# Optimization experiments

Measured on AMD Instinct MI355X. Metric: run time of the kernel, lower is better.

## Reference

```python
import jax, jax.numpy as jnp
import numpy as np

N = 20000      # nodes
E = 320000     # edges
F = 128        # feat_dim
N_RBF = 20
CUTOFF = 5.0


def setup_inputs() -> dict:
    key = jax.random.key(0)
    ks = jax.random.split(key, 12)
    h_i = jax.random.normal(ks[0], (N, F), dtype=jnp.float32)
    v_i = jax.random.normal(ks[1], (N, F, 3), dtype=jnp.float32)
    # distances in (0, cutoff); keep strictly > 0 to avoid div-by-zero in sinc basis
    d_ij = (jax.random.uniform(ks[2], (E,), dtype=jnp.float32) * 0.98 + 0.01) * CUTOFF
    r = jax.random.normal(ks[3], (E, 3), dtype=jnp.float32)
    unit_r_ij = r / jnp.linalg.norm(r, axis=-1, keepdims=True)
    nbrs = jax.random.randint(ks[4], (E, 2), 0, N, dtype=jnp.int64)
    # params: layers = Dense(F->F, swish) then Dense(F->3F); dist_embed dense: n_rbf -> 3F
    s1 = 1.0 / np.sqrt(F)
    W1 = jax.random.uniform(ks[5], (F, F), jnp.float32, -s1, s1)
    b1 = jax.random.uniform(ks[6], (F,), jnp.float32, -s1, s1)
    W2 = jax.random.uniform(ks[7], (F, 3 * F), jnp.float32, -s1, s1)
    b2 = jax.random.uniform(ks[8], (3 * F,), jnp.float32, -s1, s1)
    sr = 1.0 / np.sqrt(N_RBF)
    Wr = jax.random.uniform(ks[9], (N_RBF, 3 * F), jnp.float32, -sr, sr)
    br = jax.random.uniform(ks[10], (3 * F,), jnp.float32, -sr, sr)
    return {"h_i": h_i, "v_i": v_i, "d_ij": d_ij, "unit_r_ij": unit_r_ij,
            "nbrs": nbrs, "W1": W1, "b1": b1, "W2": W2, "b2": b2, "Wr": Wr, "br": br}


def _dist_embed(d, Wr, br):
    # PaiNN sinc-like radial basis: sin(n*pi*d/cutoff)/d, n=1..N_RBF
    n = jnp.arange(1, N_RBF + 1, dtype=d.dtype)
    rbf = jnp.sin(n[None, :] * jnp.pi * d[:, None] / CUTOFF) / d[:, None]  # [E, N_RBF]
    # cosine cutoff envelope
    fcut = 0.5 * (jnp.cos(jnp.pi * d / CUTOFF) + 1.0) * (d < CUTOFF)       # [E]
    return (rbf @ Wr + br) * fcut[:, None]                                  # [E, 3F]


def reference(h_i, v_i, d_ij, unit_r_ij, nbrs, W1, b1, W2, b2, Wr, br):
    # phi = Dense(swish) -> Dense : [N, 3F]
    phi = jax.nn.silu(h_i @ W1 + b1) @ W2 + b2
    src = nbrs[:, 1]
    dst = nbrs[:, 0]
    edge_inv = phi[src] * _dist_embed(d_ij, Wr, br)          # [E, 3F]
    edge_inv = edge_inv.reshape(edge_inv.shape[0], 3, F)     # [E, 3, F]
    f1, f2, f3 = edge_inv[:, 0], edge_inv[:, 1], edge_inv[:, 2]
    # dv: [E, F, 3]
    dv = f1[:, :, None] * unit_r_ij[:, None, :] + f2[:, :, None] * v_i[src]
    dh_i = jax.ops.segment_sum(f3, dst, num_segments=N)      # [N, F]
    dv_i = jax.ops.segment_sum(dv, dst, num_segments=N)      # [N, F, 3]
    return (dh_i, dv_i)
```

## Files before the change

kernel.cpp:

```cpp
#include <hip/hip_runtime.h>
#include <math.h>

#define F 128
#define THREEF 384
#define N_RBF 20
#define CUTOFF 5.0f
#define CAP 64

#define REP20(X) X(0) X(1) X(2) X(3) X(4) X(5) X(6) X(7) X(8) X(9) \
                 X(10) X(11) X(12) X(13) X(14) X(15) X(16) X(17) X(18) X(19)

__global__ __launch_bounds__(256) void mlp_kernel(
    const float* __restrict__ h, const float* __restrict__ W1,
    const float* __restrict__ b1, const float* __restrict__ W2,
    const float* __restrict__ b2, float* __restrict__ phi, int N)
{
    __shared__ float sh_h[16 * F];
    __shared__ float sh_t[16 * F];
    const int tid   = threadIdx.x;
    const int node0 = blockIdx.x * 16;

    {
        const float4* src = (const float4*)(h + (size_t)node0 * F);
        float4* dst = (float4*)sh_h;
        dst[tid]       = src[tid];
        dst[tid + 256] = src[tid + 256];
    }
    __syncthreads();

    const int j2 = tid & 63;
    const int r0 = (tid >> 6) * 4;

    {
        float acc[4][2];
        const float bb0 = b1[j2], bb1 = b1[j2 + 64];
        #pragma unroll
        for (int r = 0; r < 4; ++r) { acc[r][0] = bb0; acc[r][1] = bb1; }
        for (int k4 = 0; k4 < F; k4 += 4) {
            float4 a[4];
            #pragma unroll
            for (int r = 0; r < 4; ++r)
                a[r] = *(const float4*)&sh_h[(r0 + r) * F + k4];
            #pragma unroll
            for (int kk = 0; kk < 4; ++kk) {
                const float w0  = W1[(k4 + kk) * F + j2];
                const float w1v = W1[(k4 + kk) * F + j2 + 64];
                #pragma unroll
                for (int r = 0; r < 4; ++r) {
                    const float av = ((const float*)&a[r])[kk];
                    acc[r][0] = fmaf(av, w0,  acc[r][0]);
                    acc[r][1] = fmaf(av, w1v, acc[r][1]);
                }
            }
        }
        #pragma unroll
        for (int r = 0; r < 4; ++r) {
            const float x0 = acc[r][0], x1 = acc[r][1];
            sh_t[(r0 + r) * F + j2]      = x0 / (1.0f + __expf(-x0));
            sh_t[(r0 + r) * F + j2 + 64] = x1 / (1.0f + __expf(-x1));
        }
    }
    __syncthreads();

    {
        float acc[4][6];
        #pragma unroll
        for (int c = 0; c < 6; ++c) {
            const float bb = b2[j2 + c * 64];
            #pragma unroll
            for (int r = 0; r < 4; ++r) acc[r][c] = bb;
        }
        for (int k4 = 0; k4 < F; k4 += 4) {
            float4 a[4];
            #pragma unroll
            for (int r = 0; r < 4; ++r)
                a[r] = *(const float4*)&sh_t[(r0 + r) * F + k4];
            #pragma unroll
            for (int kk = 0; kk < 4; ++kk) {
                float w[6];
                #pragma unroll
                for (int c = 0; c < 6; ++c)
                    w[c] = W2[(k4 + kk) * THREEF + j2 + c * 64];
                #pragma unroll
                for (int r = 0; r < 4; ++r) {
                    const float av = ((const float*)&a[r])[kk];
                    #pragma unroll
                    for (int c = 0; c < 6; ++c)
                        acc[r][c] = fmaf(av, w[c], acc[r][c]);
                }
            }
        }
        #pragma unroll
        for (int r = 0; r < 4; ++r) {
            #pragma unroll
            for (int c = 0; c < 6; ++c) {
                const int col = j2 + c * 64;
                const int p   = col >> 7;
                const int fc  = col & 127;
                phi[(size_t)p * N * F + (size_t)(node0 + r0 + r) * F + fc] = acc[r][c];
            }
        }
    }
}

__global__ __launch_bounds__(256) void build_kernel(
    const float* __restrict__ d_ij, const float* __restrict__ unit_r,
    const int* __restrict__ nbrs, int* __restrict__ cnt,
    int* __restrict__ eid, float* __restrict__ pack, int E)
{
    int e = blockIdx.x * 256 + threadIdx.x;
    if (e >= E) return;
    const int dst = nbrs[2 * e];
    const int src = nbrs[2 * e + 1];
    const int slot = atomicAdd(&cnt[dst], 1);
    if (slot < CAP) eid[dst * CAP + slot] = e;

    const float d = d_ij[e];
    const float x = (float)M_PI * d * (1.0f / CUTOFF);
    float sx, cx;
    __sincosf(x, &sx, &cx);
    const float fcut = (d < CUTOFF) ? 0.5f * (cx + 1.0f) : 0.0f;
    float4 q0, q1;
    q0.x = sx * fcut / d;
    q0.y = 2.0f * cx;
    q0.z = fcut;
    q0.w = unit_r[3 * e + 0];
    q1.x = unit_r[3 * e + 1];
    q1.y = unit_r[3 * e + 2];
    q1.z = __int_as_float(src);
    q1.w = 0.0f;
    float4* pk = (float4*)(pack + (size_t)e * 8);
    pk[0] = q0;
    pk[1] = q1;
}

__global__ __launch_bounds__(128) void gather_kernel(
    const float* __restrict__ phi,
    const float* __restrict__ v_i,
    const float* __restrict__ Wr,
    const float* __restrict__ br,
    const int*   __restrict__ cnt,
    const int*   __restrict__ eid,
    const float* __restrict__ pack,
    float* __restrict__ dh,
    float* __restrict__ dv,
    int N)
{
    const int node = blockIdx.x;
    const int f    = threadIdx.x;

    #define DECL_WR(n) float w0_##n = Wr[(n) * THREEF + f];        \
                       float w1_##n = Wr[(n) * THREEF + f + 128];  \
                       float w2_##n = Wr[(n) * THREEF + f + 256];
    REP20(DECL_WR)
    #undef DECL_WR

    asm volatile("" : "+v"(w0_0), "+v"(w0_1), "+v"(w0_2), "+v"(w0_3),
                      "+v"(w0_4), "+v"(w0_5), "+v"(w0_6), "+v"(w0_7),
                      "+v"(w0_8), "+v"(w0_9), "+v"(w0_10), "+v"(w0_11),
                      "+v"(w0_12), "+v"(w0_13), "+v"(w0_14));
    asm volatile("" : "+v"(w0_15), "+v"(w0_16), "+v"(w0_17), "+v"(w0_18),
                      "+v"(w0_19), "+v"(w1_0), "+v"(w1_1), "+v"(w1_2),
                      "+v"(w1_3), "+v"(w1_4), "+v"(w1_5), "+v"(w1_6),
                      "+v"(w1_7), "+v"(w1_8), "+v"(w1_9));
    asm volatile("" : "+v"(w1_10), "+v"(w1_11), "+v"(w1_12), "+v"(w1_13),
                      "+v"(w1_14), "+v"(w1_15), "+v"(w1_16), "+v"(w1_17),
                      "+v"(w1_18), "+v"(w1_19), "+v"(w2_0), "+v"(w2_1),
                      "+v"(w2_2), "+v"(w2_3), "+v"(w2_4));
    asm volatile("" : "+v"(w2_5), "+v"(w2_6), "+v"(w2_7), "+v"(w2_8),
                      "+v"(w2_9), "+v"(w2_10), "+v"(w2_11), "+v"(w2_12),
                      "+v"(w2_13), "+v"(w2_14), "+v"(w2_15), "+v"(w2_16),
                      "+v"(w2_17), "+v"(w2_18), "+v"(w2_19));

    const float br0 = br[f], br1 = br[f + 128], br2 = br[f + 256];

    const int deg0 = cnt[node];
    const int deg  = deg0 < CAP ? deg0 : CAP;
    const int* my_eid = eid + node * CAP;

    const float* phi0 = phi;
    const float* phi1 = phi + (size_t)N * F;
    const float* phi2 = phi + (size_t)2 * N * F;

    float dh_acc = 0.0f, dv0 = 0.0f, dv1 = 0.0f, dv2 = 0.0f;

    for (int i = 0; i < deg; ++i) {
        const int e = __builtin_amdgcn_readfirstlane(my_eid[i]);
        const float* pk = pack + (size_t)e * 8;
        const float s1   = pk[0];
        const float twoc = pk[1];
        const float fcut = pk[2];
        const float ux   = pk[3];
        const float uy   = pk[4];
        const float uz   = pk[5];
        const int src = __builtin_amdgcn_readfirstlane(__float_as_int(pk[6]));

        float a0 = br0 * fcut, a1 = br1 * fcut, a2 = br2 * fcut;
        float rp = 0.0f, rc = s1;
        #define STEP(n) { a0 = fmaf(rc, w0_##n, a0);            \
                          a1 = fmaf(rc, w1_##n, a1);            \
                          a2 = fmaf(rc, w2_##n, a2);            \
                          const float rn = fmaf(twoc, rc, -rp); \
                          rp = rc; rc = rn; }
        REP20(STEP)
        #undef STEP

        const float f1 = phi0[(size_t)src * F + f] * a0;
        const float f2 = phi1[(size_t)src * F + f] * a1;
        const float f3 = phi2[(size_t)src * F + f] * a2;

        dh_acc += f3;

        const float* vs = v_i + (size_t)src * THREEF + 3 * f;
        dv0 = fmaf(f1, ux, fmaf(f2, vs[0], dv0));
        dv1 = fmaf(f1, uy, fmaf(f2, vs[1], dv1));
        dv2 = fmaf(f1, uz, fmaf(f2, vs[2], dv2));
    }

    dh[(size_t)node * F + f] = dh_acc;
    float* dvp = dv + (size_t)node * THREEF + 3 * f;
    dvp[0] = dv0;
    dvp[1] = dv1;
    dvp[2] = dv2;
}

extern "C" void kernel_launch(void* const* d_in, const int* in_sizes, int n_in,
                              void* d_out, int out_size, void* d_ws, size_t ws_size,
                              hipStream_t stream) {
    const float* h_i    = (const float*)d_in[0];
    const float* v_i    = (const float*)d_in[1];
    const float* d_ij   = (const float*)d_in[2];
    const float* unit_r = (const float*)d_in[3];
    const int*   nbrs   = (const int*)  d_in[4];
    const float* W1     = (const float*)d_in[5];
    const float* b1     = (const float*)d_in[6];
    const float* W2     = (const float*)d_in[7];
    const float* b2     = (const float*)d_in[8];
    const float* Wr     = (const float*)d_in[9];
    const float* br     = (const float*)d_in[10];

    const int N = in_sizes[0] / F;
    const int E = in_sizes[2];

    float* dh = (float*)d_out;
    float* dv = dh + (size_t)N * F;

    float* phi  = (float*)d_ws;
    float* pack = phi + (size_t)3 * N * F;
    int*   cnt  = (int*)(pack + (size_t)E * 8);
    int*   eid  = cnt + N;

    hipMemsetAsync(cnt, 0, (size_t)N * sizeof(int), stream);

    mlp_kernel<<<(N + 15) / 16, 256, 0, stream>>>(h_i, W1, b1, W2, b2, phi, N);
    build_kernel<<<(E + 255) / 256, 256, 0, stream>>>(d_ij, unit_r, nbrs, cnt,
                                                      eid, pack, E);
    gather_kernel<<<N, 128, 0, stream>>>(phi, v_i, Wr, br, cnt, eid, pack,
                                         dh, dv, N);
}
```

Before: 312.7 us.

## Scatter packed edge records into per-destination slots and prefetch them in gather

The build kernel now writes each edge's packed record directly into its destination node's slot array instead of writing an edge-id list, so the gather kernel reads records contiguously without an index indirection. The gather loop software-prefetches the next record as float4 loads, and launch bounds request more waves per SIMD. This trades a larger workspace (N*CAP records) and sparse scattered writes for removing the dependent eid load in the inner loop. Edges beyond CAP are still dropped, as before.

```diff
diff --git a/kernel.cpp b/kernel.cpp
--- a/kernel.cpp
+++ b/kernel.cpp
@@ -106,14 +106,14 @@
 __global__ __launch_bounds__(256) void build_kernel(
     const float* __restrict__ d_ij, const float* __restrict__ unit_r,
     const int* __restrict__ nbrs, int* __restrict__ cnt,
-    int* __restrict__ eid, float* __restrict__ pack, int E)
+    float* __restrict__ pack, int E)
 {
     int e = blockIdx.x * 256 + threadIdx.x;
     if (e >= E) return;
     const int dst = nbrs[2 * e];
     const int src = nbrs[2 * e + 1];
     const int slot = atomicAdd(&cnt[dst], 1);
-    if (slot < CAP) eid[dst * CAP + slot] = e;
+    if (slot >= CAP) return;
 
     const float d = d_ij[e];
     const float x = (float)M_PI * d * (1.0f / CUTOFF);
@@ -129,18 +129,17 @@
     q1.y = unit_r[3 * e + 2];
     q1.z = __int_as_float(src);
     q1.w = 0.0f;
-    float4* pk = (float4*)(pack + (size_t)e * 8);
+    float4* pk = (float4*)(pack + ((size_t)dst * CAP + slot) * 8);
     pk[0] = q0;
     pk[1] = q1;
 }
 
-__global__ __launch_bounds__(128) void gather_kernel(
+__global__ __launch_bounds__(128, 3) void gather_kernel(
     const float* __restrict__ phi,
     const float* __restrict__ v_i,
     const float* __restrict__ Wr,
     const float* __restrict__ br,
     const int*   __restrict__ cnt,
-    const int*   __restrict__ eid,
     const float* __restrict__ pack,
     float* __restrict__ dh,
     float* __restrict__ dv,
@@ -176,45 +175,50 @@
 
     const int deg0 = cnt[node];
     const int deg  = deg0 < CAP ? deg0 : CAP;
-    const int* my_eid = eid + node * CAP;
 
     const float* phi0 = phi;
     const float* phi1 = phi + (size_t)N * F;
     const float* phi2 = phi + (size_t)2 * N * F;
 
+    const float4* pk = (const float4*)(pack + (size_t)node * CAP * 8);
+
     float dh_acc = 0.0f, dv0 = 0.0f, dv1 = 0.0f, dv2 = 0.0f;
 
-    for (int i = 0; i < deg; ++i) {
-        const int e = __builtin_amdgcn_readfirstlane(my_eid[i]);
-        const float* pk = pack + (size_t)e * 8;
-        const float s1   = pk[0];
-        const float twoc = pk[1];
-        const float fcut = pk[2];
-        const float ux   = pk[3];
-        const float uy   = pk[4];
-        const float uz   = pk[5];
-        const int src = __builtin_amdgcn_readfirstlane(__float_as_int(pk[6]));
-
-        float a0 = br0 * fcut, a1 = br1 * fcut, a2 = br2 * fcut;
-        float rp = 0.0f, rc = s1;
-        #define STEP(n) { a0 = fmaf(rc, w0_##n, a0);            \
-                          a1 = fmaf(rc, w1_##n, a1);            \
-                          a2 = fmaf(rc, w2_##n, a2);            \
-                          const float rn = fmaf(twoc, rc, -rp); \
-                          rp = rc; rc = rn; }
-        REP20(STEP)
-        #undef STEP
-
-        const float f1 = phi0[(size_t)src * F + f] * a0;
-        const float f2 = phi1[(size_t)src * F + f] * a1;
-        const float f3 = phi2[(size_t)src * F + f] * a2;
-
-        dh_acc += f3;
-
-        const float* vs = v_i + (size_t)src * THREEF + 3 * f;
-        dv0 = fmaf(f1, ux, fmaf(f2, vs[0], dv0));
-        dv1 = fmaf(f1, uy, fmaf(f2, vs[1], dv1));
-        dv2 = fmaf(f1, uz, fmaf(f2, vs[2], dv2));
+    if (deg > 0) {
+        float4 q0 = pk[0];
+        float4 q1 = pk[1];
+        for (int i = 0; i < deg; ++i) {
+            const float4 q0n = pk[2 * i + 2];
+            const float4 q1n = pk[2 * i + 3];
+
+            const float twoc = q0.y;
+            const float fcut = q0.z;
+            const int src = __builtin_amdgcn_readfirstlane(__float_as_int(q1.z));
+
+            float a0 = br0 * fcut, a1 = br1 * fcut, a2 = br2 * fcut;
+            float rp = 0.0f, rc = q0.x;
+            #define STEP(n) { a0 = fmaf(rc, w0_##n, a0);            \
+                              a1 = fmaf(rc, w1_##n, a1);            \
+                              a2 = fmaf(rc, w2_##n, a2);            \
+                              const float rn = fmaf(twoc, rc, -rp); \
+                              rp = rc; rc = rn; }
+            REP20(STEP)
+            #undef STEP
+
+            const float f1 = phi0[(size_t)src * F + f] * a0;
+            const float f2 = phi1[(size_t)src * F + f] * a1;
+            const float f3 = phi2[(size_t)src * F + f] * a2;
+
+            dh_acc += f3;
+
+            const float* vs = v_i + (size_t)src * THREEF + 3 * f;
+            dv0 = fmaf(f1, q0.w, fmaf(f2, vs[0], dv0));
+            dv1 = fmaf(f1, q1.x, fmaf(f2, vs[1], dv1));
+            dv2 = fmaf(f1, q1.y, fmaf(f2, vs[2], dv2));
+
+            q0 = q0n;
+            q1 = q1n;
+        }
     }
 
     dh[(size_t)node * F + f] = dh_acc;
@@ -247,14 +251,13 @@
 
     float* phi  = (float*)d_ws;
     float* pack = phi + (size_t)3 * N * F;
-    int*   cnt  = (int*)(pack + (size_t)E * 8);
-    int*   eid  = cnt + N;
+    int*   cnt  = (int*)(pack + (size_t)N * CAP * 8 + 8);
 
     hipMemsetAsync(cnt, 0, (size_t)N * sizeof(int), stream);
 
     mlp_kernel<<<(N + 15) / 16, 256, 0, stream>>>(h_i, W1, b1, W2, b2, phi, N);
     build_kernel<<<(E + 255) / 256, 256, 0, stream>>>(d_ij, unit_r, nbrs, cnt,
-                                                      eid, pack, E);
-    gather_kernel<<<N, 128, 0, stream>>>(phi, v_i, Wr, br, cnt, eid, pack,
+                                                      pack, E);
+    gather_kernel<<<N, 128, 0, stream>>>(phi, v_i, Wr, br, cnt, pack,
                                          dh, dv, N);
 }
```

Measured after the change: 306.4 us. 1.02x faster.

## Batch four edges per iteration and stream Wr from cache instead of registers

Applied to the files above, without the earlier changes.

The gather kernel now processes edges in groups of four, loading their packed records and source indices up front and running the Chebyshev RBF recurrence for all four together so memory latency overlaps with arithmetic. The 60 per-thread Wr registers pinned by asm barriers are replaced with loads from global/L1 inside the RBF loop, amortized across the four edges. This trades register pressure (and possibly higher occupancy) for extra Wr loads, and masks tail edges by zeroing s1 and fcut so padded slots contribute nothing.

```diff
diff --git a/kernel.cpp b/kernel.cpp
--- a/kernel.cpp
+++ b/kernel.cpp
@@ -6,9 +6,6 @@
 #define N_RBF 20
 #define CUTOFF 5.0f
 #define CAP 64
-
-#define REP20(X) X(0) X(1) X(2) X(3) X(4) X(5) X(6) X(7) X(8) X(9) \
-                 X(10) X(11) X(12) X(13) X(14) X(15) X(16) X(17) X(18) X(19)
 
 __global__ __launch_bounds__(256) void mlp_kernel(
     const float* __restrict__ h, const float* __restrict__ W1,
@@ -149,29 +146,6 @@
     const int node = blockIdx.x;
     const int f    = threadIdx.x;
 
-    #define DECL_WR(n) float w0_##n = Wr[(n) * THREEF + f];        \
-                       float w1_##n = Wr[(n) * THREEF + f + 128];  \
-                       float w2_##n = Wr[(n) * THREEF + f + 256];
-    REP20(DECL_WR)
-    #undef DECL_WR
-
-    asm volatile("" : "+v"(w0_0), "+v"(w0_1), "+v"(w0_2), "+v"(w0_3),
-                      "+v"(w0_4), "+v"(w0_5), "+v"(w0_6), "+v"(w0_7),
-                      "+v"(w0_8), "+v"(w0_9), "+v"(w0_10), "+v"(w0_11),
-                      "+v"(w0_12), "+v"(w0_13), "+v"(w0_14));
-    asm volatile("" : "+v"(w0_15), "+v"(w0_16), "+v"(w0_17), "+v"(w0_18),
-                      "+v"(w0_19), "+v"(w1_0), "+v"(w1_1), "+v"(w1_2),
-                      "+v"(w1_3), "+v"(w1_4), "+v"(w1_5), "+v"(w1_6),
-                      "+v"(w1_7), "+v"(w1_8), "+v"(w1_9));
-    asm volatile("" : "+v"(w1_10), "+v"(w1_11), "+v"(w1_12), "+v"(w1_13),
-                      "+v"(w1_14), "+v"(w1_15), "+v"(w1_16), "+v"(w1_17),
-                      "+v"(w1_18), "+v"(w1_19), "+v"(w2_0), "+v"(w2_1),
-                      "+v"(w2_2), "+v"(w2_3), "+v"(w2_4));
-    asm volatile("" : "+v"(w2_5), "+v"(w2_6), "+v"(w2_7), "+v"(w2_8),
-                      "+v"(w2_9), "+v"(w2_10), "+v"(w2_11), "+v"(w2_12),
-                      "+v"(w2_13), "+v"(w2_14), "+v"(w2_15), "+v"(w2_16),
-                      "+v"(w2_17), "+v"(w2_18), "+v"(w2_19));
-
     const float br0 = br[f], br1 = br[f + 128], br2 = br[f + 256];
 
     const int deg0 = cnt[node];
@@ -182,39 +156,72 @@
     const float* phi1 = phi + (size_t)N * F;
     const float* phi2 = phi + (size_t)2 * N * F;
 
+    const float* wr0 = Wr + f;
+    const float* wr1 = Wr + f + 128;
+    const float* wr2 = Wr + f + 256;
+
     float dh_acc = 0.0f, dv0 = 0.0f, dv1 = 0.0f, dv2 = 0.0f;
 
-    for (int i = 0; i < deg; ++i) {
-        const int e = __builtin_amdgcn_readfirstlane(my_eid[i]);
-        const float* pk = pack + (size_t)e * 8;
-        const float s1   = pk[0];
-        const float twoc = pk[1];
-        const float fcut = pk[2];
-        const float ux   = pk[3];
-        const float uy   = pk[4];
-        const float uz   = pk[5];
-        const int src = __builtin_amdgcn_readfirstlane(__float_as_int(pk[6]));
-
-        float a0 = br0 * fcut, a1 = br1 * fcut, a2 = br2 * fcut;
-        float rp = 0.0f, rc = s1;
-        #define STEP(n) { a0 = fmaf(rc, w0_##n, a0);            \
-                          a1 = fmaf(rc, w1_##n, a1);            \
-                          a2 = fmaf(rc, w2_##n, a2);            \
-                          const float rn = fmaf(twoc, rc, -rp); \
-                          rp = rc; rc = rn; }
-        REP20(STEP)
-        #undef STEP
-
-        const float f1 = phi0[(size_t)src * F + f] * a0;
-        const float f2 = phi1[(size_t)src * F + f] * a1;
-        const float f3 = phi2[(size_t)src * F + f] * a2;
-
-        dh_acc += f3;
-
-        const float* vs = v_i + (size_t)src * THREEF + 3 * f;
-        dv0 = fmaf(f1, ux, fmaf(f2, vs[0], dv0));
-        dv1 = fmaf(f1, uy, fmaf(f2, vs[1], dv1));
-        dv2 = fmaf(f1, uz, fmaf(f2, vs[2], dv2));
+    for (int i0 = 0; i0 < deg; i0 += 4) {
+        float4 q0[4], q1[4];
+        int    srcs[4];
+
+        #pragma unroll
+        for (int j = 0; j < 4; ++j) {
+            const int idx = i0 + j;
+            const int e = __builtin_amdgcn_readfirstlane(
+                              my_eid[idx < deg ? idx : 0]);
+            const float4* pkj = (const float4*)(pack + (size_t)e * 8);
+            float4 a0 = pkj[0];
+            float4 a1 = pkj[1];
+            if (idx >= deg) { a0.x = 0.0f; a0.z = 0.0f; }
+            q0[j] = a0;
+            q1[j] = a1;
+            srcs[j] = __builtin_amdgcn_readfirstlane(__float_as_int(a1.z));
+        }
+
+        float a[4][3], rp[4], rc[4], twoc[4];
+        #pragma unroll
+        for (int j = 0; j < 4; ++j) {
+            const float fc = q0[j].z;
+            a[j][0] = br0 * fc;
+            a[j][1] = br1 * fc;
+            a[j][2] = br2 * fc;
+            rp[j]   = 0.0f;
+            rc[j]   = q0[j].x;
+            twoc[j] = q0[j].y;
+        }
+
+        #pragma unroll 4
+        for (int n = 0; n < N_RBF; ++n) {
+            const float w0 = wr0[n * THREEF];
+            const float w1 = wr1[n * THREEF];
+            const float w2 = wr2[n * THREEF];
+            #pragma unroll
+            for (int j = 0; j < 4; ++j) {
+                a[j][0] = fmaf(rc[j], w0, a[j][0]);
+                a[j][1] = fmaf(rc[j], w1, a[j][1]);
+                a[j][2] = fmaf(rc[j], w2, a[j][2]);
+                const float rn = fmaf(twoc[j], rc[j], -rp[j]);
+                rp[j] = rc[j];
+                rc[j] = rn;
+            }
+        }
+
+        #pragma unroll
+        for (int j = 0; j < 4; ++j) {
+            const int src = srcs[j];
+            const float f1 = phi0[(size_t)src * F + f] * a[j][0];
+            const float f2 = phi1[(size_t)src * F + f] * a[j][1];
+            const float f3 = phi2[(size_t)src * F + f] * a[j][2];
+
+            dh_acc += f3;
+
+            const float* vs = v_i + (size_t)src * THREEF + 3 * f;
+            dv0 = fmaf(f1, q0[j].w, fmaf(f2, vs[0], dv0));
+            dv1 = fmaf(f1, q1[j].x, fmaf(f2, vs[1], dv1));
+            dv2 = fmaf(f1, q1[j].y, fmaf(f2, vs[2], dv2));
+        }
     }
 
     dh[(size_t)node * F + f] = dh_acc;
```

After: 336.0 us. +7.5%, slower.

## Stream transposed Wr as float4 per edge instead of pinning 60 weights in registers

Applied to the files above, without the earlier changes.

Adds a small kernel that repacks Wr into float4 groups of four RBF rows per feature column. The gather kernel then reloads these weights from cache for every edge instead of holding 60 values in VGPRs, which is meant to cut register pressure and raise occupancy. The cost is 15 extra vector loads per edge iteration plus one extra tiny kernel launch. It also reads each nbrs pair as a single int2 load in the build kernel.

```diff
diff --git a/kernel.cpp b/kernel.cpp
--- a/kernel.cpp
+++ b/kernel.cpp
@@ -6,9 +6,6 @@
 #define N_RBF 20
 #define CUTOFF 5.0f
 #define CAP 64
-
-#define REP20(X) X(0) X(1) X(2) X(3) X(4) X(5) X(6) X(7) X(8) X(9) \
-                 X(10) X(11) X(12) X(13) X(14) X(15) X(16) X(17) X(18) X(19)
 
 __global__ __launch_bounds__(256) void mlp_kernel(
     const float* __restrict__ h, const float* __restrict__ W1,
@@ -103,6 +100,22 @@
     }
 }
 
+__global__ __launch_bounds__(256) void wrt_kernel(
+    const float* __restrict__ Wr, float* __restrict__ WrT)
+{
+    const int idx = blockIdx.x * 256 + threadIdx.x;
+    if (idx >= 5 * 3 * 128) return;
+    const int f  = idx & 127;
+    const int c  = (idx >> 7) % 3;
+    const int n4 = idx / (3 * 128);
+    float4 v;
+    v.x = Wr[(4 * n4 + 0) * THREEF + c * 128 + f];
+    v.y = Wr[(4 * n4 + 1) * THREEF + c * 128 + f];
+    v.z = Wr[(4 * n4 + 2) * THREEF + c * 128 + f];
+    v.w = Wr[(4 * n4 + 3) * THREEF + c * 128 + f];
+    ((float4*)WrT)[idx] = v;
+}
+
 __global__ __launch_bounds__(256) void build_kernel(
     const float* __restrict__ d_ij, const float* __restrict__ unit_r,
     const int* __restrict__ nbrs, int* __restrict__ cnt,
@@ -110,8 +123,9 @@
 {
     int e = blockIdx.x * 256 + threadIdx.x;
     if (e >= E) return;
-    const int dst = nbrs[2 * e];
-    const int src = nbrs[2 * e + 1];
+    const int2 nb = ((const int2*)nbrs)[e];
+    const int dst = nb.x;
+    const int src = nb.y;
     const int slot = atomicAdd(&cnt[dst], 1);
     if (slot < CAP) eid[dst * CAP + slot] = e;
 
@@ -137,7 +151,7 @@
 __global__ __launch_bounds__(128) void gather_kernel(
     const float* __restrict__ phi,
     const float* __restrict__ v_i,
-    const float* __restrict__ Wr,
+    const float* __restrict__ WrT,
     const float* __restrict__ br,
     const int*   __restrict__ cnt,
     const int*   __restrict__ eid,
@@ -149,29 +163,6 @@
     const int node = blockIdx.x;
     const int f    = threadIdx.x;
 
-    #define DECL_WR(n) float w0_##n = Wr[(n) * THREEF + f];        \
-                       float w1_##n = Wr[(n) * THREEF + f + 128];  \
-                       float w2_##n = Wr[(n) * THREEF + f + 256];
-    REP20(DECL_WR)
-    #undef DECL_WR
-
-    asm volatile("" : "+v"(w0_0), "+v"(w0_1), "+v"(w0_2), "+v"(w0_3),
-                      "+v"(w0_4), "+v"(w0_5), "+v"(w0_6), "+v"(w0_7),
-                      "+v"(w0_8), "+v"(w0_9), "+v"(w0_10), "+v"(w0_11),
-                      "+v"(w0_12), "+v"(w0_13), "+v"(w0_14));
-    asm volatile("" : "+v"(w0_15), "+v"(w0_16), "+v"(w0_17), "+v"(w0_18),
-                      "+v"(w0_19), "+v"(w1_0), "+v"(w1_1), "+v"(w1_2),
-                      "+v"(w1_3), "+v"(w1_4), "+v"(w1_5), "+v"(w1_6),
-                      "+v"(w1_7), "+v"(w1_8), "+v"(w1_9));
-    asm volatile("" : "+v"(w1_10), "+v"(w1_11), "+v"(w1_12), "+v"(w1_13),
-                      "+v"(w1_14), "+v"(w1_15), "+v"(w1_16), "+v"(w1_17),
-                      "+v"(w1_18), "+v"(w1_19), "+v"(w2_0), "+v"(w2_1),
-                      "+v"(w2_2), "+v"(w2_3), "+v"(w2_4));
-    asm volatile("" : "+v"(w2_5), "+v"(w2_6), "+v"(w2_7), "+v"(w2_8),
-                      "+v"(w2_9), "+v"(w2_10), "+v"(w2_11), "+v"(w2_12),
-                      "+v"(w2_13), "+v"(w2_14), "+v"(w2_15), "+v"(w2_16),
-                      "+v"(w2_17), "+v"(w2_18), "+v"(w2_19));
-
     const float br0 = br[f], br1 = br[f + 128], br2 = br[f + 256];
 
     const int deg0 = cnt[node];
@@ -181,6 +172,7 @@
     const float* phi0 = phi;
     const float* phi1 = phi + (size_t)N * F;
     const float* phi2 = phi + (size_t)2 * N * F;
+    const float4* wT  = (const float4*)WrT;
 
     float dh_acc = 0.0f, dv0 = 0.0f, dv1 = 0.0f, dv2 = 0.0f;
 
@@ -197,13 +189,24 @@
 
         float a0 = br0 * fcut, a1 = br1 * fcut, a2 = br2 * fcut;
         float rp = 0.0f, rc = s1;
-        #define STEP(n) { a0 = fmaf(rc, w0_##n, a0);            \
-                          a1 = fmaf(rc, w1_##n, a1);            \
-                          a2 = fmaf(rc, w2_##n, a2);            \
-                          const float rn = fmaf(twoc, rc, -rp); \
-                          rp = rc; rc = rn; }
-        REP20(STEP)
-        #undef STEP
+        #pragma unroll
+        for (int n4 = 0; n4 < 5; ++n4) {
+            const float4 w0 = wT[(n4 * 3 + 0) * 128 + f];
+            const float4 w1 = wT[(n4 * 3 + 1) * 128 + f];
+            const float4 w2 = wT[(n4 * 3 + 2) * 128 + f];
+            #pragma unroll
+            for (int k = 0; k < 4; ++k) {
+                const float wa = ((const float*)&w0)[k];
+                const float wb = ((const float*)&w1)[k];
+                const float wc = ((const float*)&w2)[k];
+                a0 = fmaf(rc, wa, a0);
+                a1 = fmaf(rc, wb, a1);
+                a2 = fmaf(rc, wc, a2);
+                const float rn = fmaf(twoc, rc, -rp);
+                rp = rc;
+                rc = rn;
+            }
+        }
 
         const float f1 = phi0[(size_t)src * F + f] * a0;
         const float f2 = phi1[(size_t)src * F + f] * a1;
@@ -247,14 +250,16 @@
 
     float* phi  = (float*)d_ws;
     float* pack = phi + (size_t)3 * N * F;
-    int*   cnt  = (int*)(pack + (size_t)E * 8);
+    float* WrT  = pack + (size_t)E * 8;
+    int*   cnt  = (int*)(WrT + 5 * 3 * 128 * 4);
     int*   eid  = cnt + N;
 
     hipMemsetAsync(cnt, 0, (size_t)N * sizeof(int), stream);
 
     mlp_kernel<<<(N + 15) / 16, 256, 0, stream>>>(h_i, W1, b1, W2, b2, phi, N);
+    wrt_kernel<<<8, 256, 0, stream>>>(Wr, WrT);
     build_kernel<<<(E + 255) / 256, 256, 0, stream>>>(d_ij, unit_r, nbrs, cnt,
                                                       eid, pack, E);
-    gather_kernel<<<N, 128, 0, stream>>>(phi, v_i, Wr, br, cnt, eid, pack,
+    gather_kernel<<<N, 128, 0, stream>>>(phi, v_i, WrT, br, cnt, eid, pack,
                                          dh, dv, N);
 }
```

New measurement: 310.8 us. Within noise of the previous version (-0.6%).
